# Performance work log

Measured on AMD Instinct MI355X. Metric: run time of the kernel, lower is better.

Reference implementation:

```python
import jax, jax.numpy as jnp
import numpy as np

WEIGHT = 0.1  # HISCLoss weight


def _gram(X):
    # linear kernel (the module's 'rbf' branch computes X @ Y.T)
    X = X.reshape(X.shape[0], -1)
    return X @ X.T  # [B, B]


def _center(K):
    # H K H with H = I - 11^T/B  ==  K - rowmean - colmean + grandmean
    rm = K.mean(axis=1, keepdims=True)
    cm = K.mean(axis=0, keepdims=True)
    gm = K.mean()
    return K - rm - cm + gm


def _hsic(X, Y):
    B = X.shape[0]
    Kc = _center(_gram(X))
    Lc = _center(_gram(Y))
    # trace(Kc @ Lc) without the B^3 matmul
    tr = jnp.einsum('ij,ji->', Kc, Lc)
    return tr / ((B - 1) ** 2)


def setup_inputs() -> dict:
    key = jax.random.key(0)
    ks = jax.random.split(key, 4)
    B, d = 4096, 256
    return {
        'e0': jax.random.normal(ks[0], (B, d), dtype=jnp.float32),
        'e1': jax.random.normal(ks[1], (B, d), dtype=jnp.float32),
        'e2': jax.random.normal(ks[2], (B, d), dtype=jnp.float32),
        'e3': jax.random.normal(ks[3], (B, d), dtype=jnp.float32),
    }


def reference(e0, e1, e2, e3):
    experts = [e0, e1, e2, e3]
    n = len(experts)
    vals = []
    for i in range(n):
        for j in range(i + 1, n):
            vals.append(_hsic(experts[i], experts[j]))
    L_hsic = jnp.mean(jnp.stack(vals))
    return WEIGHT * L_hsic
```

## Files before the change

### kernel.cpp

```cpp
#include <hip/hip_runtime.h>
#include <hip/hip_bf16.h>

#define B_ROWS 4096
#define DIM 256
#define NPAIR 6
#define PITCH 4160
#define BK 256
#define APITCH 264
#define KSPLIT 8
#define KCHUNK (B_ROWS / KSPLIT)

typedef short bf16x8 __attribute__((ext_vector_type(8)));
typedef float f32x4 __attribute__((ext_vector_type(4)));

__device__ __forceinline__ const float* sel(const float* e0, const float* e1,
                                            const float* e2, const float* e3, int i) {
    return i == 0 ? e0 : (i == 1 ? e1 : (i == 2 ? e2 : e3));
}

__device__ __forceinline__ int pair_i(int p) { return p < 3 ? 0 : (p < 5 ? 1 : 2); }
__device__ __forceinline__ int pair_j(int p) { return p < 3 ? p + 1 : (p < 5 ? p - 1 : 3); }

__device__ __forceinline__ unsigned short f32_to_bf16_rne(float f) {
    unsigned int u = __float_as_uint(f);
    unsigned int r = (u + 0x7FFFu + ((u >> 16) & 1u)) >> 16;
    return (unsigned short)r;
}


__global__ __launch_bounds__(256) void transpose_bf16_kernel(
        const float* __restrict__ e0, const float* __restrict__ e1,
        const float* __restrict__ e2, const float* __restrict__ e3,
        unsigned short* __restrict__ XT, float* __restrict__ sums) {
    int rt = blockIdx.x;
    int ct = blockIdx.y;
    int e  = blockIdx.z;
    const float* X = sel(e0, e1, e2, e3, e);
    unsigned short* XTe = XT + (size_t)e * DIM * PITCH;

    __shared__ float T[64][65];

    int t = threadIdx.x;
    int c4 = (t & 15) << 2;
    #pragma unroll
    for (int p = 0; p < 4; ++p) {
        int r = (t >> 4) + 16 * p;
        float4 v = *(const float4*)&X[(size_t)(rt * 64 + r) * DIM + ct * 64 + c4];
        T[c4 + 0][r] = v.x;
        T[c4 + 1][r] = v.y;
        T[c4 + 2][r] = v.z;
        T[c4 + 3][r] = v.w;
    }
    __syncthreads();

    #pragma unroll
    for (int p = 0; p < 2; ++p) {
        int id = 256 * p + t;
        int c = id >> 3;
        int roff = (id & 7) * 8;
        bf16x8 outv;
        float s8 = 0.f;
        #pragma unroll
        for (int s = 0; s < 8; ++s) {
            float f = T[c][roff + s];
            outv[s] = (short)f32_to_bf16_rne(f);
            s8 += f;
        }
        *(bf16x8*)&XTe[(size_t)(ct * 64 + c) * PITCH + rt * 64 + roff] = outv;
        s8 += __shfl_down(s8, 4, 8);
        s8 += __shfl_down(s8, 2, 8);
        s8 += __shfl_down(s8, 1, 8);
        if ((id & 7) == 0) atomicAdd(&sums[e * DIM + ct * 64 + c], s8);
    }
}

__global__ __launch_bounds__(512) void gram_v3_kernel(
        const unsigned short* __restrict__ XT, const float* __restrict__ sums,
        float* __restrict__ acc_out) {
    __shared__ __align__(16) unsigned short smem[2 * 32 * APITCH];
    unsigned short* As = smem;
    unsigned short* Bs = smem + 32 * APITCH;
    float* red = (float*)smem;

    int blk = blockIdx.x;
    int p = blk >> 6;
    int tile = blk & 63;
    int a0 = (tile >> 3) * 32;
    int b0 = (tile & 7) * 32;
    int pi = pair_i(p), pj = pair_j(p);
    const unsigned short* Xp = XT + (size_t)pi * DIM * PITCH;
    const unsigned short* Yp = XT + (size_t)pj * DIM * PITCH;

    int tid = threadIdx.x;
    int w = tid >> 6;
    int L = tid & 63;

    int srow = tid >> 5;
    int soff = (tid & 31) * 8;
    const unsigned short* gA0 = Xp + (size_t)(a0 + srow) * PITCH + soff;
    const unsigned short* gA1 = Xp + (size_t)(a0 + 16 + srow) * PITCH + soff;
    const unsigned short* gB0 = Yp + (size_t)(b0 + srow) * PITCH + soff;
    const unsigned short* gB1 = Yp + (size_t)(b0 + 16 + srow) * PITCH + soff;
    int lA0 = srow * APITCH + soff;
    int lA1 = (16 + srow) * APITCH + soff;

    bf16x8 ra0 = *(const bf16x8*)gA0;
    bf16x8 ra1 = *(const bf16x8*)gA1;
    bf16x8 rb0 = *(const bf16x8*)gB0;
    bf16x8 rb1 = *(const bf16x8*)gB1;

    f32x4 acc[2][2] = {};
    int koff = w * 32 + (L >> 4) * 8;
    int frA0 = (L & 15) * APITCH + koff;
    int frA1 = (16 + (L & 15)) * APITCH + koff;

    for (int c = 0; c < 16; ++c) {
        __syncthreads();
        *(bf16x8*)&As[lA0] = ra0;
        *(bf16x8*)&As[lA1] = ra1;
        *(bf16x8*)&Bs[lA0] = rb0;
        *(bf16x8*)&Bs[lA1] = rb1;
        int cn = (c < 15) ? (c + 1) * BK : 0;
        ra0 = *(const bf16x8*)(gA0 + cn);
        ra1 = *(const bf16x8*)(gA1 + cn);
        rb0 = *(const bf16x8*)(gB0 + cn);
        rb1 = *(const bf16x8*)(gB1 + cn);
        __syncthreads();
        bf16x8 a0f = *(const bf16x8*)&As[frA0];
        bf16x8 a1f = *(const bf16x8*)&As[frA1];
        bf16x8 b0f = *(const bf16x8*)&Bs[frA0];
        bf16x8 b1f = *(const bf16x8*)&Bs[frA1];
        acc[0][0] = __builtin_amdgcn_mfma_f32_16x16x32_bf16(a0f, b0f, acc[0][0], 0, 0, 0);
        acc[0][1] = __builtin_amdgcn_mfma_f32_16x16x32_bf16(a0f, b1f, acc[0][1], 0, 0, 0);
        acc[1][0] = __builtin_amdgcn_mfma_f32_16x16x32_bf16(a1f, b0f, acc[1][0], 0, 0, 0);
        acc[1][1] = __builtin_amdgcn_mfma_f32_16x16x32_bf16(a1f, b1f, acc[1][1], 0, 0, 0);
    }

    __syncthreads();

    #pragma unroll
    for (int ti = 0; ti < 2; ++ti)
        #pragma unroll
        for (int tj = 0; tj < 2; ++tj)
            #pragma unroll
            for (int r = 0; r < 4; ++r) {
                int m = ti * 16 + (L >> 4) * 4 + r;
                int n = tj * 16 + (L & 15);
                red[w * 1056 + m * 33 + n] = acc[ti][tj][r];
            }
    __syncthreads();

    const float inv_b = 1.0f / (float)B_ROWS;
    float local = 0.f;
    #pragma unroll
    for (int q = 0; q < 2; ++q) {
        int pos = tid + q * 512;
        int m = pos >> 5, n = pos & 31;
        float s = 0.f;
        #pragma unroll
        for (int ww = 0; ww < 8; ++ww) s += red[ww * 1056 + m * 33 + n];
        float v = s - sums[pi * DIM + a0 + m] * sums[pj * DIM + b0 + n] * inv_b;
        local = fmaf(v, v, local);
    }
    #pragma unroll
    for (int off = 32; off > 0; off >>= 1) local += __shfl_down(local, off, 64);
    __shared__ float wsum[8];
    if (L == 0) wsum[w] = local;
    __syncthreads();
    if (tid == 0) {
        float s = 0.f;
        #pragma unroll
        for (int ww = 0; ww < 8; ++ww) s += wsum[ww];
        atomicAdd(acc_out, s);
    }
}

__global__ void finalize_kernel(const float* __restrict__ acc, float* __restrict__ out) {
    if (threadIdx.x == 0) {
        const float scale = 0.1f / (6.0f * 4095.0f * 4095.0f);
        out[0] = acc[0] * scale;
    }
}


__global__ void col_sums_kernel(const float* __restrict__ e0, const float* __restrict__ e1,
                                const float* __restrict__ e2, const float* __restrict__ e3,
                                float* __restrict__ sums) {
    int e = blockIdx.y;
    const float* X = sel(e0, e1, e2, e3, e);
    int c = threadIdx.x;
    int r0 = blockIdx.x * 128;
    float s = 0.f;
    #pragma unroll 4
    for (int r = r0; r < r0 + 128; ++r) s += X[r * DIM + c];
    atomicAdd(&sums[e * DIM + c], s);
}

__global__ __launch_bounds__(256) void gram_kernel(
        const float* __restrict__ e0, const float* __restrict__ e1,
        const float* __restrict__ e2, const float* __restrict__ e3,
        float* __restrict__ G) {
    int kc = blockIdx.x;
    int tile = blockIdx.y;
    int p = blockIdx.z;
    const float* X = sel(e0, e1, e2, e3, pair_i(p));
    const float* Y = sel(e0, e1, e2, e3, pair_j(p));
    int a0 = (tile >> 2) * 64;
    int b0 = (tile & 3) * 64;
    int k0 = kc * KCHUNK;
    __shared__ float As[16][64];
    __shared__ float Bs[16][64];
    int lid = threadIdx.x;
    int lr = lid >> 4;
    int lc = (lid & 15) << 2;
    int ty = lid >> 4;
    int tx = lid & 15;
    float acc[4][4] = {};
    for (int ks = 0; ks < KCHUNK; ks += 16) {
        int row = k0 + ks + lr;
        float4 av = *(const float4*)&X[row * DIM + a0 + lc];
        float4 bv = *(const float4*)&Y[row * DIM + b0 + lc];
        __syncthreads();
        *(float4*)&As[lr][lc] = av;
        *(float4*)&Bs[lr][lc] = bv;
        __syncthreads();
        #pragma unroll
        for (int k = 0; k < 16; ++k) {
            float a[4], b[4];
            *(float4*)a = *(const float4*)&As[k][ty * 4];
            *(float4*)b = *(const float4*)&Bs[k][tx * 4];
            #pragma unroll
            for (int i = 0; i < 4; ++i)
                #pragma unroll
                for (int j = 0; j < 4; ++j)
                    acc[i][j] = fmaf(a[i], b[j], acc[i][j]);
        }
    }
    float* Gp = G + p * (DIM * DIM);
    #pragma unroll
    for (int i = 0; i < 4; ++i)
        #pragma unroll
        for (int j = 0; j < 4; ++j)
            atomicAdd(&Gp[(a0 + ty * 4 + i) * DIM + (b0 + tx * 4 + j)], acc[i][j]);
}

__global__ void reduce_kernel(const float* __restrict__ G, const float* __restrict__ sums,
                              float* __restrict__ acc) {
    float local = 0.f;
    const int total = NPAIR * DIM * DIM;
    for (int idx = blockIdx.x * blockDim.x + threadIdx.x; idx < total;
         idx += gridDim.x * blockDim.x) {
        int p = idx >> 16;
        int ab = idx & 65535;
        int a = ab >> 8;
        int b = ab & 255;
        float v = G[idx] - sums[pair_i(p) * DIM + a] * sums[pair_j(p) * DIM + b] * (1.0f / (float)B_ROWS);
        local = fmaf(v, v, local);
    }
    #pragma unroll
    for (int off = 32; off > 0; off >>= 1) local += __shfl_down(local, off, 64);
    __shared__ float wsum[4];
    if ((threadIdx.x & 63) == 0) wsum[threadIdx.x >> 6] = local;
    __syncthreads();
    if (threadIdx.x == 0) {
        float s = wsum[0] + wsum[1] + wsum[2] + wsum[3];
        atomicAdd(acc, s);
    }
}


extern "C" void kernel_launch(void* const* d_in, const int* in_sizes, int n_in,
                              void* d_out, int out_size, void* d_ws, size_t ws_size,
                              hipStream_t stream) {
    const float* e0 = (const float*)d_in[0];
    const float* e1 = (const float*)d_in[1];
    const float* e2 = (const float*)d_in[2];
    const float* e3 = (const float*)d_in[3];

    float* sums = (float*)d_ws;
    float* acc  = (float*)((char*)d_ws + 4096);
    size_t need = 8192 + (size_t)4 * DIM * PITCH * sizeof(unsigned short);

    if (ws_size >= need) {
        unsigned short* XT = (unsigned short*)((char*)d_ws + 8192);
        hipMemsetAsync(d_ws, 0, 8192, stream);
        transpose_bf16_kernel<<<dim3(64, 4, 4), 256, 0, stream>>>(e0, e1, e2, e3, XT, sums);
        gram_v3_kernel<<<NPAIR * 64, 512, 0, stream>>>(XT, sums, acc);
        finalize_kernel<<<1, 64, 0, stream>>>(acc, (float*)d_out);
    } else {
        float* G = (float*)((char*)d_ws + 8192);
        size_t zbytes = 8192 + (size_t)NPAIR * DIM * DIM * sizeof(float);
        hipMemsetAsync(d_ws, 0, zbytes, stream);
        col_sums_kernel<<<dim3(32, 4), 256, 0, stream>>>(e0, e1, e2, e3, sums);
        gram_kernel<<<dim3(KSPLIT, 16, NPAIR), 256, 0, stream>>>(e0, e1, e2, e3, G);
        reduce_kernel<<<384, 256, 0, stream>>>(G, sums, acc);
        finalize_kernel<<<1, 64, 0, stream>>>(acc, (float*)d_out);
    }
}
```

Before: 91.60 us.

## Halve gram tile width to double block count and fuse finalize via ticket counter

Splits each 32x32 cross-gram output tile into 32x16 tiles, so the launch grows from 384 to 768 blocks across the 256x256 output per pair, giving better CU occupancy on the MI355X. Each block now issues two MFMAs per K chunk instead of four, and loads less B data. The separate finalize kernel is removed: the last block, identified by an atomic ticket counter, scales the accumulated sum and writes the output. This saves a kernel launch but rereads A tiles twice as often.

Measured after the change: 109.1 us. +19.1%, slower.

```diff
diff --git a/kernel.cpp b/kernel.cpp
--- a/kernel.cpp
+++ b/kernel.cpp
@@ -74,19 +74,20 @@
     }
 }
 
-__global__ __launch_bounds__(512) void gram_v3_kernel(
+__global__ __launch_bounds__(512) void gram_v5_kernel(
         const unsigned short* __restrict__ XT, const float* __restrict__ sums,
-        float* __restrict__ acc_out) {
-    __shared__ __align__(16) unsigned short smem[2 * 32 * APITCH];
+        float* __restrict__ acc_out, unsigned int* __restrict__ counter,
+        float* __restrict__ out) {
+    __shared__ __align__(16) unsigned short smem[48 * APITCH];
     unsigned short* As = smem;
     unsigned short* Bs = smem + 32 * APITCH;
     float* red = (float*)smem;
 
     int blk = blockIdx.x;
-    int p = blk >> 6;
-    int tile = blk & 63;
-    int a0 = (tile >> 3) * 32;
-    int b0 = (tile & 7) * 32;
+    int p = blk >> 7;
+    int tile = blk & 127;
+    int a0 = (tile >> 4) * 32;
+    int b0 = (tile & 15) * 16;
     int pi = pair_i(p), pj = pair_j(p);
     const unsigned short* Xp = XT + (size_t)pi * DIM * PITCH;
     const unsigned short* Yp = XT + (size_t)pj * DIM * PITCH;
@@ -99,79 +100,74 @@
     int soff = (tid & 31) * 8;
     const unsigned short* gA0 = Xp + (size_t)(a0 + srow) * PITCH + soff;
     const unsigned short* gA1 = Xp + (size_t)(a0 + 16 + srow) * PITCH + soff;
-    const unsigned short* gB0 = Yp + (size_t)(b0 + srow) * PITCH + soff;
-    const unsigned short* gB1 = Yp + (size_t)(b0 + 16 + srow) * PITCH + soff;
+    const unsigned short* gB  = Yp + (size_t)(b0 + srow) * PITCH + soff;
     int lA0 = srow * APITCH + soff;
     int lA1 = (16 + srow) * APITCH + soff;
+    int lB  = srow * APITCH + soff;
 
     bf16x8 ra0 = *(const bf16x8*)gA0;
     bf16x8 ra1 = *(const bf16x8*)gA1;
-    bf16x8 rb0 = *(const bf16x8*)gB0;
-    bf16x8 rb1 = *(const bf16x8*)gB1;
-
-    f32x4 acc[2][2] = {};
+    bf16x8 rb  = *(const bf16x8*)gB;
+
+    f32x4 acc0 = {}, acc1 = {};
     int koff = w * 32 + (L >> 4) * 8;
-    int frA0 = (L & 15) * APITCH + koff;
-    int frA1 = (16 + (L & 15)) * APITCH + koff;
+    int fA0 = (L & 15) * APITCH + koff;
+    int fA1 = (16 + (L & 15)) * APITCH + koff;
+    int fB  = (L & 15) * APITCH + koff;
 
     for (int c = 0; c < 16; ++c) {
         __syncthreads();
         *(bf16x8*)&As[lA0] = ra0;
         *(bf16x8*)&As[lA1] = ra1;
-        *(bf16x8*)&Bs[lA0] = rb0;
-        *(bf16x8*)&Bs[lA1] = rb1;
+        *(bf16x8*)&Bs[lB]  = rb;
         int cn = (c < 15) ? (c + 1) * BK : 0;
         ra0 = *(const bf16x8*)(gA0 + cn);
         ra1 = *(const bf16x8*)(gA1 + cn);
-        rb0 = *(const bf16x8*)(gB0 + cn);
-        rb1 = *(const bf16x8*)(gB1 + cn);
-        __syncthreads();
-        bf16x8 a0f = *(const bf16x8*)&As[frA0];
-        bf16x8 a1f = *(const bf16x8*)&As[frA1];
-        bf16x8 b0f = *(const bf16x8*)&Bs[frA0];
-        bf16x8 b1f = *(const bf16x8*)&Bs[frA1];
-        acc[0][0] = __builtin_amdgcn_mfma_f32_16x16x32_bf16(a0f, b0f, acc[0][0], 0, 0, 0);
-        acc[0][1] = __builtin_amdgcn_mfma_f32_16x16x32_bf16(a0f, b1f, acc[0][1], 0, 0, 0);
-        acc[1][0] = __builtin_amdgcn_mfma_f32_16x16x32_bf16(a1f, b0f, acc[1][0], 0, 0, 0);
-        acc[1][1] = __builtin_amdgcn_mfma_f32_16x16x32_bf16(a1f, b1f, acc[1][1], 0, 0, 0);
-    }
-
-    __syncthreads();
-
-    #pragma unroll
-    for (int ti = 0; ti < 2; ++ti)
-        #pragma unroll
-        for (int tj = 0; tj < 2; ++tj)
-            #pragma unroll
-            for (int r = 0; r < 4; ++r) {
-                int m = ti * 16 + (L >> 4) * 4 + r;
-                int n = tj * 16 + (L & 15);
-                red[w * 1056 + m * 33 + n] = acc[ti][tj][r];
-            }
+        rb  = *(const bf16x8*)(gB + cn);
+        __syncthreads();
+        bf16x8 a0f = *(const bf16x8*)&As[fA0];
+        bf16x8 a1f = *(const bf16x8*)&As[fA1];
+        bf16x8 b0f = *(const bf16x8*)&Bs[fB];
+        acc0 = __builtin_amdgcn_mfma_f32_16x16x32_bf16(a0f, b0f, acc0, 0, 0, 0);
+        acc1 = __builtin_amdgcn_mfma_f32_16x16x32_bf16(a1f, b0f, acc1, 0, 0, 0);
+    }
+
+    __syncthreads();
+
+    #pragma unroll
+    for (int r = 0; r < 4; ++r) {
+        int m = (L >> 4) * 4 + r;
+        int n = L & 15;
+        red[w * 544 + m * 17 + n] = acc0[r];
+        red[w * 544 + (16 + m) * 17 + n] = acc1[r];
+    }
     __syncthreads();
 
     const float inv_b = 1.0f / (float)B_ROWS;
-    float local = 0.f;
-    #pragma unroll
-    for (int q = 0; q < 2; ++q) {
-        int pos = tid + q * 512;
-        int m = pos >> 5, n = pos & 31;
-        float s = 0.f;
-        #pragma unroll
-        for (int ww = 0; ww < 8; ++ww) s += red[ww * 1056 + m * 33 + n];
-        float v = s - sums[pi * DIM + a0 + m] * sums[pj * DIM + b0 + n] * inv_b;
-        local = fmaf(v, v, local);
-    }
+    int m = tid >> 4, n = tid & 15;
+    float s = 0.f;
+    #pragma unroll
+    for (int ww = 0; ww < 8; ++ww) s += red[ww * 544 + m * 17 + n];
+    float v = s - sums[pi * DIM + a0 + m] * sums[pj * DIM + b0 + n] * inv_b;
+    float local = v * v;
+
     #pragma unroll
     for (int off = 32; off > 0; off >>= 1) local += __shfl_down(local, off, 64);
     __shared__ float wsum[8];
     if (L == 0) wsum[w] = local;
     __syncthreads();
     if (tid == 0) {
-        float s = 0.f;
-        #pragma unroll
-        for (int ww = 0; ww < 8; ++ww) s += wsum[ww];
-        atomicAdd(acc_out, s);
+        float bsum = 0.f;
+        #pragma unroll
+        for (int ww = 0; ww < 8; ++ww) bsum += wsum[ww];
+        atomicAdd(acc_out, bsum);
+        __threadfence();
+        unsigned int tkt = atomicAdd(counter, 1u);
+        if (tkt == (unsigned int)(gridDim.x - 1)) {
+            float total = atomicAdd(acc_out, 0.0f);
+            const float scale = 0.1f / (6.0f * 4095.0f * 4095.0f);
+            out[0] = total * scale;
+        }
     }
 }
 
@@ -279,14 +275,14 @@
 
     float* sums = (float*)d_ws;
     float* acc  = (float*)((char*)d_ws + 4096);
+    unsigned int* counter = (unsigned int*)((char*)d_ws + 4160);
     size_t need = 8192 + (size_t)4 * DIM * PITCH * sizeof(unsigned short);
 
     if (ws_size >= need) {
         unsigned short* XT = (unsigned short*)((char*)d_ws + 8192);
         hipMemsetAsync(d_ws, 0, 8192, stream);
         transpose_bf16_kernel<<<dim3(64, 4, 4), 256, 0, stream>>>(e0, e1, e2, e3, XT, sums);
-        gram_v3_kernel<<<NPAIR * 64, 512, 0, stream>>>(XT, sums, acc);
-        finalize_kernel<<<1, 64, 0, stream>>>(acc, (float*)d_out);
+        gram_v5_kernel<<<NPAIR * 128, 512, 0, stream>>>(XT, sums, acc, counter, (float*)d_out);
     } else {
         float* G = (float*)((char*)d_ws + 8192);
         size_t zbytes = 8192 + (size_t)NPAIR * DIM * DIM * sizeof(float);
```

## Fuse column sums and finalize into gram kernel with last-block ticket

Applied to the files above, without the earlier changes.

Removes the atomic column-sum accumulation from the transpose kernel and instead computes per-row sums of the bf16 transposed data inside the gram kernel while staging tiles. The separate finalize launch is replaced by a ticket counter so the last block writes the scaled result, and the memset shrinks. This saves one kernel launch and many global atomics, but the sums now come from bf16-rounded values rather than fp32 inputs, which slightly changes accuracy.

Measured after the change: 94.70 us. +3.4%, slower.

```diff
diff --git a/kernel.cpp b/kernel.cpp
--- a/kernel.cpp
+++ b/kernel.cpp
@@ -27,11 +27,22 @@
     return (unsigned short)r;
 }
 
+__device__ __forceinline__ float bf16_to_f32(short h) {
+    return __uint_as_float(((unsigned int)(unsigned short)h) << 16);
+}
+
+__device__ __forceinline__ float sum8(bf16x8 v) {
+    float s = 0.f;
+    #pragma unroll
+    for (int k = 0; k < 8; ++k) s += bf16_to_f32(v[k]);
+    return s;
+}
+
 
 __global__ __launch_bounds__(256) void transpose_bf16_kernel(
         const float* __restrict__ e0, const float* __restrict__ e1,
         const float* __restrict__ e2, const float* __restrict__ e3,
-        unsigned short* __restrict__ XT, float* __restrict__ sums) {
+        unsigned short* __restrict__ XT) {
     int rt = blockIdx.x;
     int ct = blockIdx.y;
     int e  = blockIdx.z;
@@ -59,28 +70,23 @@
         int c = id >> 3;
         int roff = (id & 7) * 8;
         bf16x8 outv;
-        float s8 = 0.f;
-        #pragma unroll
-        for (int s = 0; s < 8; ++s) {
-            float f = T[c][roff + s];
-            outv[s] = (short)f32_to_bf16_rne(f);
-            s8 += f;
-        }
+        #pragma unroll
+        for (int s = 0; s < 8; ++s)
+            outv[s] = (short)f32_to_bf16_rne(T[c][roff + s]);
         *(bf16x8*)&XTe[(size_t)(ct * 64 + c) * PITCH + rt * 64 + roff] = outv;
-        s8 += __shfl_down(s8, 4, 8);
-        s8 += __shfl_down(s8, 2, 8);
-        s8 += __shfl_down(s8, 1, 8);
-        if ((id & 7) == 0) atomicAdd(&sums[e * DIM + ct * 64 + c], s8);
-    }
-}
-
-__global__ __launch_bounds__(512) void gram_v3_kernel(
-        const unsigned short* __restrict__ XT, const float* __restrict__ sums,
-        float* __restrict__ acc_out) {
+    }
+}
+
+__global__ __launch_bounds__(512) void gram_v6_kernel(
+        const unsigned short* __restrict__ XT,
+        float* __restrict__ acc_out, unsigned int* __restrict__ counter,
+        float* __restrict__ out) {
     __shared__ __align__(16) unsigned short smem[2 * 32 * APITCH];
     unsigned short* As = smem;
     unsigned short* Bs = smem + 32 * APITCH;
     float* red = (float*)smem;
+    __shared__ float Sx[32], Sy[32];
+    __shared__ float wsum[8];
 
     int blk = blockIdx.x;
     int p = blk >> 6;
@@ -110,6 +116,7 @@
     bf16x8 rb1 = *(const bf16x8*)gB1;
 
     f32x4 acc[2][2] = {};
+    float sa0 = 0.f, sa1 = 0.f, sb0 = 0.f, sb1 = 0.f;
     int koff = w * 32 + (L >> 4) * 8;
     int frA0 = (L & 15) * APITCH + koff;
     int frA1 = (16 + (L & 15)) * APITCH + koff;
@@ -120,6 +127,8 @@
         *(bf16x8*)&As[lA1] = ra1;
         *(bf16x8*)&Bs[lA0] = rb0;
         *(bf16x8*)&Bs[lA1] = rb1;
+        sa0 += sum8(ra0); sa1 += sum8(ra1);
+        sb0 += sum8(rb0); sb1 += sum8(rb1);
         int cn = (c < 15) ? (c + 1) * BK : 0;
         ra0 = *(const bf16x8*)(gA0 + cn);
         ra1 = *(const bf16x8*)(gA1 + cn);
@@ -139,6 +148,18 @@
     __syncthreads();
 
     #pragma unroll
+    for (int off = 16; off > 0; off >>= 1) {
+        sa0 += __shfl_down(sa0, off, 32);
+        sa1 += __shfl_down(sa1, off, 32);
+        sb0 += __shfl_down(sb0, off, 32);
+        sb1 += __shfl_down(sb1, off, 32);
+    }
+    if ((tid & 31) == 0) {
+        Sx[srow] = sa0; Sx[16 + srow] = sa1;
+        Sy[srow] = sb0; Sy[16 + srow] = sb1;
+    }
+
+    #pragma unroll
     for (int ti = 0; ti < 2; ++ti)
         #pragma unroll
         for (int tj = 0; tj < 2; ++tj)
@@ -159,19 +180,26 @@
         float s = 0.f;
         #pragma unroll
         for (int ww = 0; ww < 8; ++ww) s += red[ww * 1056 + m * 33 + n];
-        float v = s - sums[pi * DIM + a0 + m] * sums[pj * DIM + b0 + n] * inv_b;
+        float v = s - Sx[m] * Sy[n] * inv_b;
         local = fmaf(v, v, local);
     }
     #pragma unroll
     for (int off = 32; off > 0; off >>= 1) local += __shfl_down(local, off, 64);
-    __shared__ float wsum[8];
     if (L == 0) wsum[w] = local;
     __syncthreads();
     if (tid == 0) {
-        float s = 0.f;
-        #pragma unroll
-        for (int ww = 0; ww < 8; ++ww) s += wsum[ww];
-        atomicAdd(acc_out, s);
+        float bsum = 0.f;
+        #pragma unroll
+        for (int ww = 0; ww < 8; ++ww) bsum += wsum[ww];
+        atomicAdd(acc_out, bsum);
+        __threadfence();
+        unsigned int tkt = atomicAdd(counter, 1u);
+        if (tkt == (unsigned int)(gridDim.x - 1)) {
+            __threadfence();
+            float total = atomicAdd(acc_out, 0.0f);
+            const float scale = 0.1f / (6.0f * 4095.0f * 4095.0f);
+            out[0] = total * scale;
+        }
     }
 }
 
@@ -279,14 +307,14 @@
 
     float* sums = (float*)d_ws;
     float* acc  = (float*)((char*)d_ws + 4096);
+    unsigned int* counter = (unsigned int*)((char*)d_ws + 4160);
     size_t need = 8192 + (size_t)4 * DIM * PITCH * sizeof(unsigned short);
 
     if (ws_size >= need) {
         unsigned short* XT = (unsigned short*)((char*)d_ws + 8192);
-        hipMemsetAsync(d_ws, 0, 8192, stream);
-        transpose_bf16_kernel<<<dim3(64, 4, 4), 256, 0, stream>>>(e0, e1, e2, e3, XT, sums);
-        gram_v3_kernel<<<NPAIR * 64, 512, 0, stream>>>(XT, sums, acc);
-        finalize_kernel<<<1, 64, 0, stream>>>(acc, (float*)d_out);
+        hipMemsetAsync((char*)d_ws + 4096, 0, 128, stream);
+        transpose_bf16_kernel<<<dim3(64, 4, 4), 256, 0, stream>>>(e0, e1, e2, e3, XT);
+        gram_v6_kernel<<<NPAIR * 64, 512, 0, stream>>>(XT, acc, counter, (float*)d_out);
     } else {
         float* G = (float*)((char*)d_ws + 8192);
         size_t zbytes = 8192 + (size_t)NPAIR * DIM * DIM * sizeof(float);
```
